# Performance work log

Hardware: AMD Instinct MI355X
Metric: run time of the kernel (lower is better)

The kernel has to match this reference:

```python
import jax, jax.numpy as jnp
import numpy as np

DT = 0.1  # module init arg dt


def _skew(v):
    x, y, z = v[..., 0], v[..., 1], v[..., 2]
    o = jnp.zeros_like(x)
    return jnp.stack([
        jnp.stack([o, -z, y], -1),
        jnp.stack([z, o, -x], -1),
        jnp.stack([-y, x, o], -1)], -2)


def _se3_exp(xi):
    # pypose se3 convention: [tau (trans), phi (rot)]
    tau, phi = xi[..., :3], xi[..., 3:6]
    th2 = jnp.sum(phi * phi, -1)
    th = jnp.sqrt(th2)
    small = th < 1e-4
    ts = jnp.where(small, 1.0, th)
    A = jnp.where(small, 1.0 - th2 / 6.0, jnp.sin(ts) / ts)
    B = jnp.where(small, 0.5 - th2 / 24.0, (1.0 - jnp.cos(ts)) / (ts * ts))
    C = jnp.where(small, 1.0 / 6.0 - th2 / 120.0, (ts - jnp.sin(ts)) / (ts ** 3))
    K = _skew(phi)
    K2 = K @ K
    I = jnp.eye(3, dtype=xi.dtype)
    R = I + A[..., None, None] * K + B[..., None, None] * K2
    V = I + B[..., None, None] * K + C[..., None, None] * K2
    t = jnp.einsum('...ij,...j->...i', V, tau)
    return R, t


def _so3_log(R):
    tr = R[..., 0, 0] + R[..., 1, 1] + R[..., 2, 2]
    c = jnp.clip((tr - 1.0) * 0.5, -1.0 + 1e-7, 1.0 - 1e-7)
    th = jnp.arccos(c)
    small = th < 1e-4
    ts = jnp.where(small, 1.0, th)
    coef = jnp.where(small, 0.5 + th * th / 12.0, ts / (2.0 * jnp.sin(ts)))
    W = coef[..., None, None] * (R - jnp.swapaxes(R, -1, -2))
    return jnp.stack([W[..., 2, 1], W[..., 0, 2], W[..., 1, 0]], -1), th


def _se3_log(R, t):
    phi, th = _so3_log(R)
    th2 = th * th
    small = th < 1e-4
    ts = jnp.where(small, 1.0, th)
    # V^{-1} coefficient: (1 - th*sin(th)/(2*(1-cos(th))))/th^2, Taylor 1/12 + th^2/720
    D = jnp.where(small, 1.0 / 12.0 + th2 / 720.0,
                  (1.0 - ts * jnp.sin(ts) / (2.0 * (1.0 - jnp.cos(ts)))) / (ts * ts))
    K = _skew(phi)
    K2 = K @ K
    I = jnp.eye(3, dtype=R.dtype)
    Vinv = I - 0.5 * K + D[..., None, None] * K2
    tau = jnp.einsum('...ij,...j->...i', Vinv, t)
    return jnp.concatenate([tau, phi], -1)


def _compose(a, b):
    Ra, ta = a
    Rb, tb = b
    return Ra @ Rb, jnp.einsum('...ij,...j->...i', Ra, tb) + ta


def _inv(a):
    R, t = a
    Rt = jnp.swapaxes(R, -1, -2)
    return Rt, -jnp.einsum('...ij,...j->...i', Rt, t)


def _kinematic_consistency(x, dt):
    x_t = x[..., :-1, :]
    x_t_dt = x[..., 1:, :]
    H_t = _se3_exp(x_t[..., :6])
    fwd = _compose(_se3_exp(x_t[..., 6:] * (dt / 2.0)), H_t)
    H_t_dt = _se3_exp(x_t_dt[..., :6])
    bwd = _compose(_se3_exp(x_t_dt[..., 6:] * (-dt / 2.0)), H_t_dt)
    Rd, td = _compose(fwd, _inv(bwd))
    xi = _se3_log(Rd, td)
    return jnp.linalg.norm(xi, axis=-1)  # [B, H-1]


def setup_inputs() -> dict:
    key = jax.random.key(0)
    k1, k2, k3, k4 = jax.random.split(key, 4)
    traj = jax.random.normal(k1, (8192, 128, 12), jnp.float32)
    k = jax.random.randint(k2, (8192,), 0, 1000)
    t_weights = jax.random.uniform(k3, (127,), jnp.float32)
    k_weights = jax.random.uniform(k4, (1000,), jnp.float32)
    return {"traj": traj, "k": k, "t_weights": t_weights, "k_weights": k_weights}


def reference(traj, k, t_weights, k_weights):
    score = _kinematic_consistency(traj, DT)
    loss = score * score  # mse vs zeros, reduction='none'
    weighted = (loss * t_weights).mean(axis=1) * k_weights[k]  # [B]
    return weighted.mean()
```

## Files before the change

### kernel.cpp

```cpp
#include <hip/hip_runtime.h>
#include <math.h>

#define DEV __device__ __forceinline__

DEV float fast_rcp(float x) { return __builtin_amdgcn_rcpf(x); }

DEV float fast_acos(float x) {
    float ax = fabsf(x);
    float p = fmaf(ax, -0.0187293f, 0.0742610f);
    p = fmaf(ax, p, -0.2121144f);
    p = fmaf(ax, p, 1.5707288f);
    float r = sqrtf(1.0f - ax) * p;
    return (x < 0.0f) ? (3.14159265358979f - r) : r;
}

DEV void se3_exp(float tau0, float tau1, float tau2,
                 float x, float y, float z,
                 float R[9], float t[3]) {
    float th2 = x*x + y*y + z*z;
    float th  = sqrtf(th2);
    bool small = th < 1e-4f;
    float ts  = small ? 1.0f : th;
    float s   = __sinf(ts);
    float c   = __cosf(ts);
    float inv = fast_rcp(ts);
    float A = small ? (1.0f - th2 * (1.0f/6.0f))      : s * inv;
    float B = small ? (0.5f - th2 * (1.0f/24.0f))     : (1.0f - c) * inv * inv;
    float C = small ? (1.0f/6.0f - th2*(1.0f/120.0f)) : (ts - s) * inv * inv * inv;

    float Bxy = B*x*y, Bxz = B*x*z, Byz = B*y*z;
    R[0] = 1.0f - B*(y*y + z*z);
    R[1] = Bxy - A*z;
    R[2] = Bxz + A*y;
    R[3] = Bxy + A*z;
    R[4] = 1.0f - B*(x*x + z*z);
    R[5] = Byz - A*x;
    R[6] = Bxz - A*y;
    R[7] = Byz + A*x;
    R[8] = 1.0f - B*(x*x + y*y);

    float Cxy = C*x*y, Cxz = C*x*z, Cyz = C*y*z;
    float V0 = 1.0f - C*(y*y + z*z);
    float V1 = Cxy - B*z;
    float V2 = Cxz + B*y;
    float V3 = Cxy + B*z;
    float V4 = 1.0f - C*(x*x + z*z);
    float V5 = Cyz - B*x;
    float V6 = Cxz - B*y;
    float V7 = Cyz + B*x;
    float V8 = 1.0f - C*(x*x + y*y);
    t[0] = V0*tau0 + V1*tau1 + V2*tau2;
    t[1] = V3*tau0 + V4*tau1 + V5*tau2;
    t[2] = V6*tau0 + V7*tau1 + V8*tau2;
}

__global__ __launch_bounds__(128)
void kin_kernel(const float* __restrict__ traj, const int* __restrict__ kidx,
                const float* __restrict__ tw, const float* __restrict__ kw,
                float* __restrict__ partial) {
    __shared__ float bS[128 * 13];
    __shared__ float wsum[2];
    const int b   = blockIdx.x;
    const int tid = threadIdx.x;

    const float* row = traj + (size_t)b * 1536 + tid * 12;
    float4 v0 = *(const float4*)(row + 0);
    float4 v1 = *(const float4*)(row + 4);
    float4 v2 = *(const float4*)(row + 8);
    float tweight = (tid < 127) ? tw[tid] : 0.0f;

    float Rp[9], tp[3], Rv[9], tv[3];
    se3_exp(v0.x, v0.y, v0.z, v0.w, v1.x, v1.y, Rp, tp);
    const float h = 0.05f;
    se3_exp(v1.z*h, v1.w*h, v2.x*h, v2.y*h, v2.z*h, v2.w*h, Rv, tv);

    float F[12];
    float* g = &bS[tid * 13];
    #pragma unroll
    for (int i = 0; i < 3; i++) {
        #pragma unroll
        for (int j = 0; j < 3; j++) {
            F[i*3+j]  = Rv[i*3+0]*Rp[0*3+j] + Rv[i*3+1]*Rp[1*3+j] + Rv[i*3+2]*Rp[2*3+j];
            g[i*3+j]  = Rv[0*3+i]*Rp[0*3+j] + Rv[1*3+i]*Rp[1*3+j] + Rv[2*3+i]*Rp[2*3+j];
        }
    }
    float d0 = tp[0] - tv[0], d1 = tp[1] - tv[1], d2 = tp[2] - tv[2];
    #pragma unroll
    for (int i = 0; i < 3; i++) {
        F[9+i] = Rv[i*3+0]*tp[0] + Rv[i*3+1]*tp[1] + Rv[i*3+2]*tp[2] + tv[i];
        g[9+i] = Rv[0*3+i]*d0 + Rv[1*3+i]*d1 + Rv[2*3+i]*d2;
    }
    __syncthreads();

    float term = 0.0f;
    if (tid < 127) {
        const float* B = &bS[(tid + 1) * 13];
        float Rd[9];
        #pragma unroll
        for (int i = 0; i < 3; i++)
            #pragma unroll
            for (int j = 0; j < 3; j++)
                Rd[i*3+j] = F[i*3+0]*B[j*3+0] + F[i*3+1]*B[j*3+1] + F[i*3+2]*B[j*3+2];
        float td0 = F[9]  - (Rd[0]*B[9] + Rd[1]*B[10] + Rd[2]*B[11]);
        float td1 = F[10] - (Rd[3]*B[9] + Rd[4]*B[10] + Rd[5]*B[11]);
        float td2 = F[11] - (Rd[6]*B[9] + Rd[7]*B[10] + Rd[8]*B[11]);

        float tr = Rd[0] + Rd[4] + Rd[8];
        float c  = fminf(fmaxf((tr - 1.0f) * 0.5f, -1.0f + 1e-7f), 1.0f - 1e-7f);
        float th = fast_acos(c);
        float sn = sqrtf(fmaxf(1.0f - c*c, 1e-20f));
        float coef = th * fast_rcp(2.0f * sn);
        float px = coef * (Rd[7] - Rd[5]);
        float py = coef * (Rd[2] - Rd[6]);
        float pz = coef * (Rd[3] - Rd[1]);

        float D = (1.0f - th*sn*fast_rcp(2.0f*(1.0f - c))) * fast_rcp(th*th);
        float Dxy = D*px*py, Dxz = D*px*pz, Dyz = D*py*pz;
        float Vi0 = 1.0f - D*(py*py + pz*pz);
        float Vi1 = Dxy + 0.5f*pz;
        float Vi2 = Dxz - 0.5f*py;
        float Vi3 = Dxy - 0.5f*pz;
        float Vi4 = 1.0f - D*(px*px + pz*pz);
        float Vi5 = Dyz + 0.5f*px;
        float Vi6 = Dxz + 0.5f*py;
        float Vi7 = Dyz - 0.5f*px;
        float Vi8 = 1.0f - D*(px*px + py*py);
        float ux = Vi0*td0 + Vi1*td1 + Vi2*td2;
        float uy = Vi3*td0 + Vi4*td1 + Vi5*td2;
        float uz = Vi6*td0 + Vi7*td1 + Vi8*td2;

        float loss = ux*ux + uy*uy + uz*uz + px*px + py*py + pz*pz;
        term = loss * tweight;
    }

    float v = term;
    #pragma unroll
    for (int off = 32; off; off >>= 1) v += __shfl_down(v, off, 64);
    if ((tid & 63) == 0) wsum[tid >> 6] = v;
    __syncthreads();
    if (tid == 0)
        partial[b] = (wsum[0] + wsum[1]) * kw[kidx[b]];
}

__global__ __launch_bounds__(256)
void reduce_kernel(const float* __restrict__ partial, float* __restrict__ out, int n) {
    __shared__ float ws[4];
    int tid = threadIdx.x;
    float v = 0.0f;
    for (int i = tid; i < n; i += 256) v += partial[i];
    #pragma unroll
    for (int off = 32; off; off >>= 1) v += __shfl_down(v, off, 64);
    if ((tid & 63) == 0) ws[tid >> 6] = v;
    __syncthreads();
    if (tid == 0)
        out[0] = (ws[0] + ws[1] + ws[2] + ws[3]) * (1.0f / (127.0f * 8192.0f));
}

extern "C" void kernel_launch(void* const* d_in, const int* in_sizes, int n_in,
                              void* d_out, int out_size, void* d_ws, size_t ws_size,
                              hipStream_t stream) {
    const float* traj = (const float*)d_in[0];
    const int*   k    = (const int*)d_in[1];
    const float* tw   = (const float*)d_in[2];
    const float* kw   = (const float*)d_in[3];
    float* out     = (float*)d_out;
    float* partial = (float*)d_ws;
    const int B = in_sizes[1];

    kin_kernel<<<B, 128, 0, stream>>>(traj, k, tw, kw, partial);
    reduce_kernel<<<1, 256, 0, stream>>>(partial, out, B);
}
```

Before: 101.9 us.

## Map one trajectory per wavefront with two timesteps per lane and shuffle exchange

Each 64-lane wavefront now handles one whole trajectory, and each lane processes two consecutive timesteps. The neighbour's backward transform comes from a cross-lane shuffle instead of LDS, which removes the shared-memory staging and both block-level barriers. Blocks hold four trajectories, and the final reduction reads the partials as float4 using 512 threads. In exchange there is more register pressure per lane and less parallelism, and the code assumes B is a multiple of 4.

```diff
diff --git a/kernel.cpp b/kernel.cpp
--- a/kernel.cpp
+++ b/kernel.cpp
@@ -54,106 +54,127 @@
     t[2] = V6*tau0 + V7*tau1 + V8*tau2;
 }
 
-__global__ __launch_bounds__(128)
+DEV void make_fwd_bwd(const float Rp[9], const float tp[3],
+                      const float Rv[9], const float tv[3],
+                      float F[12], float Bw[12]) {
+    #pragma unroll
+    for (int i = 0; i < 3; i++)
+        #pragma unroll
+        for (int j = 0; j < 3; j++) {
+            F[i*3+j]  = Rv[i*3+0]*Rp[0*3+j] + Rv[i*3+1]*Rp[1*3+j] + Rv[i*3+2]*Rp[2*3+j];
+            Bw[i*3+j] = Rv[0*3+i]*Rp[0*3+j] + Rv[1*3+i]*Rp[1*3+j] + Rv[2*3+i]*Rp[2*3+j];
+        }
+    float d0 = tp[0]-tv[0], d1 = tp[1]-tv[1], d2 = tp[2]-tv[2];
+    #pragma unroll
+    for (int i = 0; i < 3; i++) {
+        F[9+i]  = Rv[i*3+0]*tp[0] + Rv[i*3+1]*tp[1] + Rv[i*3+2]*tp[2] + tv[i];
+        Bw[9+i] = Rv[0*3+i]*d0 + Rv[1*3+i]*d1 + Rv[2*3+i]*d2;
+    }
+}
+
+DEV float pair_loss(const float F[12], const float B[12]) {
+    float Rd[9];
+    #pragma unroll
+    for (int i = 0; i < 3; i++)
+        #pragma unroll
+        for (int j = 0; j < 3; j++)
+            Rd[i*3+j] = F[i*3+0]*B[j*3+0] + F[i*3+1]*B[j*3+1] + F[i*3+2]*B[j*3+2];
+    float td0 = F[9]  - (Rd[0]*B[9] + Rd[1]*B[10] + Rd[2]*B[11]);
+    float td1 = F[10] - (Rd[3]*B[9] + Rd[4]*B[10] + Rd[5]*B[11]);
+    float td2 = F[11] - (Rd[6]*B[9] + Rd[7]*B[10] + Rd[8]*B[11]);
+
+    float tr = Rd[0] + Rd[4] + Rd[8];
+    float c  = fminf(fmaxf((tr - 1.0f) * 0.5f, -1.0f + 1e-7f), 1.0f - 1e-7f);
+    float th = fast_acos(c);
+    float sn = sqrtf(fmaxf(1.0f - c*c, 1e-20f));
+    float coef = th * fast_rcp(2.0f * sn);
+    float px = coef * (Rd[7] - Rd[5]);
+    float py = coef * (Rd[2] - Rd[6]);
+    float pz = coef * (Rd[3] - Rd[1]);
+
+    float D = (1.0f - th*sn*fast_rcp(2.0f*(1.0f - c))) * fast_rcp(th*th);
+    float Dxy = D*px*py, Dxz = D*px*pz, Dyz = D*py*pz;
+    float Vi0 = 1.0f - D*(py*py + pz*pz);
+    float Vi1 = Dxy + 0.5f*pz;
+    float Vi2 = Dxz - 0.5f*py;
+    float Vi3 = Dxy - 0.5f*pz;
+    float Vi4 = 1.0f - D*(px*px + pz*pz);
+    float Vi5 = Dyz + 0.5f*px;
+    float Vi6 = Dxz + 0.5f*py;
+    float Vi7 = Dyz - 0.5f*px;
+    float Vi8 = 1.0f - D*(px*px + py*py);
+    float ux = Vi0*td0 + Vi1*td1 + Vi2*td2;
+    float uy = Vi3*td0 + Vi4*td1 + Vi5*td2;
+    float uz = Vi6*td0 + Vi7*td1 + Vi8*td2;
+
+    return ux*ux + uy*uy + uz*uz + px*px + py*py + pz*pz;
+}
+
+__global__ __launch_bounds__(256)
 void kin_kernel(const float* __restrict__ traj, const int* __restrict__ kidx,
                 const float* __restrict__ tw, const float* __restrict__ kw,
                 float* __restrict__ partial) {
-    __shared__ float bS[128 * 13];
-    __shared__ float wsum[2];
-    const int b   = blockIdx.x;
-    const int tid = threadIdx.x;
+    const int tid     = threadIdx.x;
+    const int lane    = tid & 63;
+    const int traj_id = blockIdx.x * 4 + (tid >> 6);
 
-    const float* row = traj + (size_t)b * 1536 + tid * 12;
-    float4 v0 = *(const float4*)(row + 0);
-    float4 v1 = *(const float4*)(row + 4);
-    float4 v2 = *(const float4*)(row + 8);
-    float tweight = (tid < 127) ? tw[tid] : 0.0f;
+    const float* base = traj + (size_t)traj_id * 1536 + lane * 24;
+    float4 a0 = *(const float4*)(base + 0);
+    float4 a1 = *(const float4*)(base + 4);
+    float4 a2 = *(const float4*)(base + 8);
+    float4 b0 = *(const float4*)(base + 12);
+    float4 b1 = *(const float4*)(base + 16);
+    float4 b2 = *(const float4*)(base + 20);
 
+    float kwv = kw[kidx[traj_id]];
+    float w0  = tw[2*lane];
+    float w1  = (lane < 63) ? tw[2*lane + 1] : 0.0f;
+
+    const float h = 0.05f;
     float Rp[9], tp[3], Rv[9], tv[3];
-    se3_exp(v0.x, v0.y, v0.z, v0.w, v1.x, v1.y, Rp, tp);
-    const float h = 0.05f;
-    se3_exp(v1.z*h, v1.w*h, v2.x*h, v2.y*h, v2.z*h, v2.w*h, Rv, tv);
 
-    float F[12];
-    float* g = &bS[tid * 13];
+    se3_exp(a0.x,a0.y,a0.z, a0.w,a1.x,a1.y, Rp, tp);
+    se3_exp(a1.z*h,a1.w*h,a2.x*h, a2.y*h,a2.z*h,a2.w*h, Rv, tv);
+    float FA[12], BA[12];
+    make_fwd_bwd(Rp,tp,Rv,tv, FA,BA);
+
+    float RB[12];
     #pragma unroll
-    for (int i = 0; i < 3; i++) {
-        #pragma unroll
-        for (int j = 0; j < 3; j++) {
-            F[i*3+j]  = Rv[i*3+0]*Rp[0*3+j] + Rv[i*3+1]*Rp[1*3+j] + Rv[i*3+2]*Rp[2*3+j];
-            g[i*3+j]  = Rv[0*3+i]*Rp[0*3+j] + Rv[1*3+i]*Rp[1*3+j] + Rv[2*3+i]*Rp[2*3+j];
-        }
-    }
-    float d0 = tp[0] - tv[0], d1 = tp[1] - tv[1], d2 = tp[2] - tv[2];
+    for (int i = 0; i < 12; i++) RB[i] = __shfl_down(BA[i], 1, 64);
+
+    se3_exp(b0.x,b0.y,b0.z, b0.w,b1.x,b1.y, Rp, tp);
+    se3_exp(b1.z*h,b1.w*h,b2.x*h, b2.y*h,b2.z*h,b2.w*h, Rv, tv);
+    float FB[12], BB[12];
+    make_fwd_bwd(Rp,tp,Rv,tv, FB,BB);
+
+    float term = pair_loss(FA, BB) * w0;
+    if (lane < 63) term += pair_loss(FB, RB) * w1;
+
     #pragma unroll
-    for (int i = 0; i < 3; i++) {
-        F[9+i] = Rv[i*3+0]*tp[0] + Rv[i*3+1]*tp[1] + Rv[i*3+2]*tp[2] + tv[i];
-        g[9+i] = Rv[0*3+i]*d0 + Rv[1*3+i]*d1 + Rv[2*3+i]*d2;
-    }
-    __syncthreads();
-
-    float term = 0.0f;
-    if (tid < 127) {
-        const float* B = &bS[(tid + 1) * 13];
-        float Rd[9];
-        #pragma unroll
-        for (int i = 0; i < 3; i++)
-            #pragma unroll
-            for (int j = 0; j < 3; j++)
-                Rd[i*3+j] = F[i*3+0]*B[j*3+0] + F[i*3+1]*B[j*3+1] + F[i*3+2]*B[j*3+2];
-        float td0 = F[9]  - (Rd[0]*B[9] + Rd[1]*B[10] + Rd[2]*B[11]);
-        float td1 = F[10] - (Rd[3]*B[9] + Rd[4]*B[10] + Rd[5]*B[11]);
-        float td2 = F[11] - (Rd[6]*B[9] + Rd[7]*B[10] + Rd[8]*B[11]);
-
-        float tr = Rd[0] + Rd[4] + Rd[8];
-        float c  = fminf(fmaxf((tr - 1.0f) * 0.5f, -1.0f + 1e-7f), 1.0f - 1e-7f);
-        float th = fast_acos(c);
-        float sn = sqrtf(fmaxf(1.0f - c*c, 1e-20f));
-        float coef = th * fast_rcp(2.0f * sn);
-        float px = coef * (Rd[7] - Rd[5]);
-        float py = coef * (Rd[2] - Rd[6]);
-        float pz = coef * (Rd[3] - Rd[1]);
-
-        float D = (1.0f - th*sn*fast_rcp(2.0f*(1.0f - c))) * fast_rcp(th*th);
-        float Dxy = D*px*py, Dxz = D*px*pz, Dyz = D*py*pz;
-        float Vi0 = 1.0f - D*(py*py + pz*pz);
-        float Vi1 = Dxy + 0.5f*pz;
-        float Vi2 = Dxz - 0.5f*py;
-        float Vi3 = Dxy - 0.5f*pz;
-        float Vi4 = 1.0f - D*(px*px + pz*pz);
-        float Vi5 = Dyz + 0.5f*px;
-        float Vi6 = Dxz + 0.5f*py;
-        float Vi7 = Dyz - 0.5f*px;
-        float Vi8 = 1.0f - D*(px*px + py*py);
-        float ux = Vi0*td0 + Vi1*td1 + Vi2*td2;
-        float uy = Vi3*td0 + Vi4*td1 + Vi5*td2;
-        float uz = Vi6*td0 + Vi7*td1 + Vi8*td2;
-
-        float loss = ux*ux + uy*uy + uz*uz + px*px + py*py + pz*pz;
-        term = loss * tweight;
-    }
-
-    float v = term;
-    #pragma unroll
-    for (int off = 32; off; off >>= 1) v += __shfl_down(v, off, 64);
-    if ((tid & 63) == 0) wsum[tid >> 6] = v;
-    __syncthreads();
-    if (tid == 0)
-        partial[b] = (wsum[0] + wsum[1]) * kw[kidx[b]];
+    for (int off = 32; off; off >>= 1) term += __shfl_down(term, off, 64);
+    if (lane == 0) partial[traj_id] = term * kwv;
 }
 
-__global__ __launch_bounds__(256)
-void reduce_kernel(const float* __restrict__ partial, float* __restrict__ out, int n) {
-    __shared__ float ws[4];
+__global__ __launch_bounds__(512)
+void reduce_kernel(const float4* __restrict__ partial4, float* __restrict__ out,
+                   int n4, float scale) {
+    __shared__ float ws[8];
     int tid = threadIdx.x;
     float v = 0.0f;
-    for (int i = tid; i < n; i += 256) v += partial[i];
+    for (int i = tid; i < n4; i += 512) {
+        float4 p = partial4[i];
+        v += (p.x + p.y) + (p.z + p.w);
+    }
     #pragma unroll
     for (int off = 32; off; off >>= 1) v += __shfl_down(v, off, 64);
     if ((tid & 63) == 0) ws[tid >> 6] = v;
     __syncthreads();
-    if (tid == 0)
-        out[0] = (ws[0] + ws[1] + ws[2] + ws[3]) * (1.0f / (127.0f * 8192.0f));
+    if (tid == 0) {
+        float s = 0.0f;
+        #pragma unroll
+        for (int i = 0; i < 8; i++) s += ws[i];
+        out[0] = s * scale;
+    }
 }
 
 extern "C" void kernel_launch(void* const* d_in, const int* in_sizes, int n_in,
@@ -167,6 +188,7 @@
     float* partial = (float*)d_ws;
     const int B = in_sizes[1];
 
-    kin_kernel<<<B, 128, 0, stream>>>(traj, k, tw, kw, partial);
-    reduce_kernel<<<1, 256, 0, stream>>>(partial, out, B);
+    kin_kernel<<<B / 4, 256, 0, stream>>>(traj, k, tw, kw, partial);
+    float scale = 1.0f / (127.0f * (float)B);
+    reduce_kernel<<<1, 512, 0, stream>>>((const float4*)partial, out, B / 4, scale);
 }
```

Result: faster. 96.05 us (-5.7%).
